# Optimization experiments

Measured on AMD Instinct MI355X. Metric: run time of the kernel, lower is better.

Reference implementation:

```python
import jax, jax.numpy as jnp
import numpy as np

B = 65536
PEP, TCR, D, FF = 384, 480, 128, 512
H1, H2, OUT = 128, 64, 1
EPS = 1e-5


def _ln(x, g, b):
    mu = jnp.mean(x, axis=-1, keepdims=True)
    var = jnp.mean((x - mu) ** 2, axis=-1, keepdims=True)
    return (x - mu) * jax.lax.rsqrt(var + EPS) * g + b


def _bn(x, g, b):
    # training-mode BatchNorm1d: batch-wide stats, biased variance
    mu = jnp.mean(x, axis=0, keepdims=True)
    var = jnp.mean((x - mu) ** 2, axis=0, keepdims=True)
    return (x - mu) * jax.lax.rsqrt(var + EPS) * g + b


def setup_inputs() -> dict:
    key = jax.random.key(0)
    ks = iter(jax.random.split(key, 40))

    def w(shape, fan):
        s = float(np.sqrt(6.0 / fan))
        return jax.random.uniform(next(ks), shape, jnp.float32, -s, s)

    inp = {
        "x": jax.random.normal(next(ks), (B, PEP + TCR), jnp.float32),
        "w_pep": w((D, PEP), PEP + D), "b_pep": jnp.zeros(D),
        "w_tcr": w((D, TCR), TCR + D), "b_tcr": jnp.zeros(D),
        "wv_p2t": w((D, D), 2 * D), "bv_p2t": jnp.zeros(D),
        "wo_p2t": w((D, D), 2 * D), "bo_p2t": jnp.zeros(D),
        "wv_t2p": w((D, D), 2 * D), "bv_t2p": jnp.zeros(D),
        "wo_t2p": w((D, D), 2 * D), "bo_t2p": jnp.zeros(D),
        "ln_g1p": jnp.ones(D), "ln_b1p": jnp.zeros(D),
        "ln_g2p": jnp.ones(D), "ln_b2p": jnp.zeros(D),
        "ln_g1t": jnp.ones(D), "ln_b1t": jnp.zeros(D),
        "ln_g2t": jnp.ones(D), "ln_b2t": jnp.zeros(D),
        "ffn_w1p": w((FF, D), D + FF), "ffn_b1p": jnp.zeros(FF),
        "ffn_w2p": w((D, FF), D + FF), "ffn_b2p": jnp.zeros(D),
        "ffn_w1t": w((FF, D), D + FF), "ffn_b1t": jnp.zeros(FF),
        "ffn_w2t": w((D, FF), D + FF), "ffn_b2t": jnp.zeros(D),
        "w_h1": w((H1, 2 * D), 2 * D + H1), "b_h1": jnp.zeros(H1),
        "bn1_g": jnp.ones(H1), "bn1_b": jnp.zeros(H1),
        "w_h2": w((H2, H1), H1 + H2), "b_h2": jnp.zeros(H2),
        "bn2_g": jnp.ones(H2), "bn2_b": jnp.zeros(H2),
        "w_out": w((OUT, H2), H2 + OUT), "b_out": jnp.zeros(OUT),
    }
    return inp


def reference(x, w_pep, b_pep, w_tcr, b_tcr,
              wv_p2t, bv_p2t, wo_p2t, bo_p2t,
              wv_t2p, bv_t2p, wo_t2p, bo_t2p,
              ln_g1p, ln_b1p, ln_g2p, ln_b2p,
              ln_g1t, ln_b1t, ln_g2t, ln_b2t,
              ffn_w1p, ffn_b1p, ffn_w2p, ffn_b2p,
              ffn_w1t, ffn_b1t, ffn_w2t, ffn_b2t,
              w_h1, b_h1, bn1_g, bn1_b,
              w_h2, b_h2, bn2_g, bn2_b,
              w_out, b_out):
    pep = x[:, :PEP] @ w_pep.T + b_pep   # (B, 128)
    tcr = x[:, PEP:] @ w_tcr.T + b_tcr   # (B, 128)

    # MHA with seq_len=1: softmax over single key == 1 exactly,
    # so attention output = out_proj(v_proj(key/value input)).
    pa = (tcr @ wv_p2t.T + bv_p2t) @ wo_p2t.T + bo_p2t
    pa = _ln(pep + pa, ln_g1p, ln_b1p)
    h = jax.nn.gelu(pa @ ffn_w1p.T + ffn_b1p, approximate=False)
    pa = _ln(pa + h @ ffn_w2p.T + ffn_b2p, ln_g2p, ln_b2p)

    ta = (pep @ wv_t2p.T + bv_t2p) @ wo_t2p.T + bo_t2p
    ta = _ln(tcr + ta, ln_g1t, ln_b1t)
    h = jax.nn.gelu(ta @ ffn_w1t.T + ffn_b1t, approximate=False)
    ta = _ln(ta + h @ ffn_w2t.T + ffn_b2t, ln_g2t, ln_b2t)

    combined = jnp.concatenate([pa, ta], axis=1)  # (B, 256)
    h1 = jax.nn.gelu(_bn(combined @ w_h1.T + b_h1, bn1_g, bn1_b), approximate=False)
    h2 = jax.nn.gelu(_bn(h1 @ w_h2.T + b_h2, bn2_g, bn2_b), approximate=False)
    return h2 @ w_out.T + b_out  # (B, 1)
```

## Files before the change

### kernel.cpp

```cpp
#include <hip/hip_runtime.h>
#include <hip/hip_bf16.h>
#include <math.h>


typedef __attribute__((ext_vector_type(8))) __bf16 bf16x8;
typedef __attribute__((ext_vector_type(8))) short s16x8;
typedef __attribute__((ext_vector_type(4))) float f32x4;

union S8U { s16x8 s; bf16x8 b; };

__device__ __forceinline__ short f2b(float f) {
  union { float f; unsigned u; } v; v.f = f;
  unsigned r = v.u + 0x7fffu + ((v.u >> 16) & 1u);
  return (short)(r >> 16);
}
__device__ __forceinline__ float b2f(short s) {
  union { unsigned u; float f; } v; v.u = ((unsigned)(unsigned short)s) << 16;
  return v.f;
}
__device__ __forceinline__ float gelu_f(float x) {
  return 0.5f * x * (1.0f + erff(x * 0.7071067811865475f));
}

template<int NTS>
__device__ __forceinline__ void mfma_step(const short* __restrict__ Abuf, int lda, int kkA,
                                          const short* __restrict__ W, int ldw, int kw,
                                          int colbase, int l16, int q,
                                          f32x4 (&acc)[4][NTS]) {
  S8U a[4];
#pragma unroll
  for (int mt = 0; mt < 4; ++mt)
    a[mt].s = *(const s16x8*)(Abuf + (16 * mt + l16) * lda + kkA + 8 * q);
#pragma unroll
  for (int nt = 0; nt < NTS; ++nt) {
    S8U b;
    b.s = *(const s16x8*)(W + (size_t)(colbase + 16 * nt + l16) * ldw + kw + 8 * q);
#pragma unroll
    for (int mt = 0; mt < 4; ++mt)
      acc[mt][nt] = __builtin_amdgcn_mfma_f32_16x16x32_bf16(a[mt].b, b.b, acc[mt][nt], 0, 0, 0);
  }
}

template<int NTS>
__device__ __forceinline__ void zero_acc(f32x4 (&acc)[4][NTS]) {
  f32x4 z = {0.f, 0.f, 0.f, 0.f};
#pragma unroll
  for (int mt = 0; mt < 4; ++mt)
#pragma unroll
    for (int nt = 0; nt < NTS; ++nt) acc[mt][nt] = z;
}

__device__ __forceinline__ void epi_bias_store(f32x4 (&acc)[4][2], const float* __restrict__ bias,
                                               short* dst, int w, int l16, int q, bool do_gelu) {
#pragma unroll
  for (int nt = 0; nt < 2; ++nt) {
    int col = 32 * w + 16 * nt + l16;
    float bb = bias[col];
#pragma unroll
    for (int mt = 0; mt < 4; ++mt)
#pragma unroll
      for (int r = 0; r < 4; ++r) {
        int row = 16 * mt + 4 * q + r;
        float v = acc[mt][nt][r] + bb;
        if (do_gelu) v = gelu_f(v);
        dst[row * 136 + col] = f2b(v);
      }
  }
}

__device__ __forceinline__ void epi_res_ln(f32x4 (&acc)[4][2], const float* __restrict__ bias,
                                           const short* resbuf,
                                           const float* __restrict__ g, const float* __restrict__ bta,
                                           short* dst, float (*lnp)[4][2], float (*murs)[2],
                                           int w, int l16, int q, int tid) {
#pragma unroll
  for (int nt = 0; nt < 2; ++nt) {
    int col = 32 * w + 16 * nt + l16;
    float bb = bias[col];
#pragma unroll
    for (int mt = 0; mt < 4; ++mt)
#pragma unroll
      for (int r = 0; r < 4; ++r) {
        int row = 16 * mt + 4 * q + r;
        acc[mt][nt][r] += bb + b2f(resbuf[row * 136 + col]);
      }
  }
#pragma unroll
  for (int mt = 0; mt < 4; ++mt) {
#pragma unroll
    for (int r = 0; r < 4; ++r) {
      float v0 = acc[mt][0][r], v1 = acc[mt][1][r];
      float s = v0 + v1;
      float sq = v0 * v0 + v1 * v1;
#pragma unroll
      for (int off = 1; off < 16; off <<= 1) {
        s += __shfl_xor(s, off);
        sq += __shfl_xor(sq, off);
      }
      if (l16 == 0) {
        int row = 16 * mt + 4 * q + r;
        lnp[row][w][0] = s;
        lnp[row][w][1] = sq;
      }
    }
  }
  __syncthreads();
  if (tid < 64) {
    float s = lnp[tid][0][0] + lnp[tid][1][0] + lnp[tid][2][0] + lnp[tid][3][0];
    float sq = lnp[tid][0][1] + lnp[tid][1][1] + lnp[tid][2][1] + lnp[tid][3][1];
    float mu = s * (1.0f / 128.0f);
    float var = sq * (1.0f / 128.0f) - mu * mu;
    murs[tid][0] = mu;
    murs[tid][1] = rsqrtf(var + 1e-5f);
  }
  __syncthreads();
#pragma unroll
  for (int nt = 0; nt < 2; ++nt) {
    int col = 32 * w + 16 * nt + l16;
    float gg = g[col], b2 = bta[col];
#pragma unroll
    for (int mt = 0; mt < 4; ++mt)
#pragma unroll
      for (int r = 0; r < 4; ++r) {
        int row = 16 * mt + 4 * q + r;
        float v = (acc[mt][nt][r] - murs[row][0]) * murs[row][1] * gg + b2;
        dst[row * 136 + col] = f2b(v);
      }
  }
}

__device__ __forceinline__ void ffn_block(const short* __restrict__ w1, const short* __restrict__ w2,
                                          const float* __restrict__ b1, const float* __restrict__ b2,
                                          const float* __restrict__ g, const float* __restrict__ bta,
                                          short* act, short* H,
                                          float (*lnp)[4][2], float (*murs)[2],
                                          int w, int l16, int q, int tid) {
  f32x4 acc2[4][2];
  zero_acc(acc2);
  for (int c = 0; c < 4; ++c) {
    f32x4 acch[4][2];
    zero_acc(acch);
#pragma unroll
    for (int kk = 0; kk < 4; ++kk)
      mfma_step<2>(act, 136, 32 * kk, w1, 128, 32 * kk, c * 128 + 32 * w, l16, q, acch);
#pragma unroll
    for (int nt = 0; nt < 2; ++nt) {
      int lcol = 32 * w + 16 * nt + l16;
      float bb = b1[c * 128 + lcol];
#pragma unroll
      for (int mt = 0; mt < 4; ++mt)
#pragma unroll
        for (int r = 0; r < 4; ++r)
          H[(16 * mt + 4 * q + r) * 136 + lcol] = f2b(gelu_f(acch[mt][nt][r] + bb));
    }
    __syncthreads();
#pragma unroll
    for (int kk = 0; kk < 4; ++kk)
      mfma_step<2>(H, 136, 32 * kk, w2, 512, c * 128 + 32 * kk, 32 * w, l16, q, acc2);
    __syncthreads();
  }
  epi_res_ln(acc2, b2, act, g, bta, act, lnp, murs, w, l16, q, tid);
}

struct K1Args {
  const float* x;
  const short *wpep, *wtcr, *wvp, *wop, *wvt, *wot, *w1p, *w2p, *w1t, *w2t, *wh1;
  const float *bpep, *btcr, *bvp, *bop, *bvt, *bot;
  const float *g1p, *e1p, *g2p, *e2p, *g1t, *e1t, *g2t, *e2t;
  const float *b1p, *b2p, *b1t, *b2t, *bh1;
  float *sum1, *sq1;
  short* h1;
};

__global__ __launch_bounds__(256, 2) void k1_main(K1Args A) {
  __shared__ __align__(16) short smem[4 * 64 * 136 + 2 * 64 * 40];
  short* U = smem;
  short* V = U + 64 * 136;
  short* T = V + 64 * 136;
  short* H = T + 64 * 136;
  short* S = H + 64 * 136;
  float (*lnp)[4][2] = (float (*)[4][2])(void*)S;
  float (*murs)[2] = (float (*)[2])(void*)(S + 1024);

  const int tid = threadIdx.x;
  const int w = tid >> 6;
  const int lane = tid & 63;
  const int l16 = lane & 15;
  const int q = lane >> 4;
  const size_t row0 = (size_t)blockIdx.x * 64;

  auto stage = [&](int kbase, short* Sb) {
    int r = tid >> 2, c8 = (tid & 3) * 8;
    const float* p = A.x + (row0 + r) * 864 + kbase + c8;
    float4 f0 = *(const float4*)p;
    float4 f1 = *(const float4*)(p + 4);
    s16x8 o;
    o[0] = f2b(f0.x); o[1] = f2b(f0.y); o[2] = f2b(f0.z); o[3] = f2b(f0.w);
    o[4] = f2b(f1.x); o[5] = f2b(f1.y); o[6] = f2b(f1.z); o[7] = f2b(f1.w);
    *(s16x8*)(Sb + r * 40 + c8) = o;
  };

  f32x4 acc[4][2];

  zero_acc(acc);
  for (int t = 0; t < 12; ++t) {
    stage(32 * t, S + (t & 1) * (64 * 40));
    __syncthreads();
    mfma_step<2>(S + (t & 1) * (64 * 40), 40, 0, A.wpep, 384, 32 * t, 32 * w, l16, q, acc);
  }
  epi_bias_store(acc, A.bpep, U, w, l16, q, false);

  zero_acc(acc);
  for (int t = 0; t < 15; ++t) {
    stage(384 + 32 * t, S + (t & 1) * (64 * 40));
    __syncthreads();
    mfma_step<2>(S + (t & 1) * (64 * 40), 40, 0, A.wtcr, 480, 32 * t, 32 * w, l16, q, acc);
  }
  epi_bias_store(acc, A.btcr, V, w, l16, q, false);
  __syncthreads();

  zero_acc(acc);
#pragma unroll
  for (int kk = 0; kk < 4; ++kk)
    mfma_step<2>(V, 136, 32 * kk, A.wvp, 128, 32 * kk, 32 * w, l16, q, acc);
  epi_bias_store(acc, A.bvp, T, w, l16, q, false);

  zero_acc(acc);
#pragma unroll
  for (int kk = 0; kk < 4; ++kk)
    mfma_step<2>(U, 136, 32 * kk, A.wvt, 128, 32 * kk, 32 * w, l16, q, acc);
  epi_bias_store(acc, A.bvt, H, w, l16, q, false);
  __syncthreads();

  zero_acc(acc);
#pragma unroll
  for (int kk = 0; kk < 4; ++kk)
    mfma_step<2>(T, 136, 32 * kk, A.wop, 128, 32 * kk, 32 * w, l16, q, acc);
  epi_res_ln(acc, A.bop, U, A.g1p, A.e1p, U, lnp, murs, w, l16, q, tid);

  zero_acc(acc);
#pragma unroll
  for (int kk = 0; kk < 4; ++kk)
    mfma_step<2>(H, 136, 32 * kk, A.wot, 128, 32 * kk, 32 * w, l16, q, acc);
  epi_res_ln(acc, A.bot, V, A.g1t, A.e1t, V, lnp, murs, w, l16, q, tid);

  ffn_block(A.w1p, A.w2p, A.b1p, A.b2p, A.g2p, A.e2p, U, H, lnp, murs, w, l16, q, tid);
  ffn_block(A.w1t, A.w2t, A.b1t, A.b2t, A.g2t, A.e2t, V, H, lnp, murs, w, l16, q, tid);
  __syncthreads();

  zero_acc(acc);
#pragma unroll
  for (int s = 0; s < 8; ++s)
    mfma_step<2>((s < 4) ? U : V, 136, 32 * (s & 3), A.wh1, 256, 32 * s, 32 * w, l16, q, acc);
#pragma unroll
  for (int nt = 0; nt < 2; ++nt) {
    int col = 32 * w + 16 * nt + l16;
    float bb = A.bh1[col];
    float s = 0.f, sq = 0.f;
#pragma unroll
    for (int mt = 0; mt < 4; ++mt)
#pragma unroll
      for (int r = 0; r < 4; ++r) {
        float v = acc[mt][nt][r] + bb;
        s += v; sq += v * v;
        A.h1[(row0 + 16 * mt + 4 * q + r) * 128 + col] = f2b(v);
      }
    s += __shfl_xor(s, 16); sq += __shfl_xor(sq, 16);
    s += __shfl_xor(s, 32); sq += __shfl_xor(sq, 32);
    if (q == 0) {
      atomicAdd(&A.sum1[col], s);
      atomicAdd(&A.sq1[col], sq);
    }
  }
}

struct K2Args {
  const short* h1;
  const short* wh2;
  const float *bh2, *bn1g, *bn1b;
  const float *sum1, *sq1;
  float *sum2, *sq2;
  short* h2;
};

__global__ __launch_bounds__(256) void k2_main(K2Args A) {
  __shared__ __align__(16) short S2[64 * 136];
  __shared__ float s1[128], t1[128];
  const int tid = threadIdx.x;
  const int w = tid >> 6, lane = tid & 63, l16 = lane & 15, q = lane >> 4;
  const size_t row0 = (size_t)blockIdx.x * 64;

  if (tid < 128) {
    float su = A.sum1[tid], sq = A.sq1[tid];
    float mu = su * (1.0f / 65536.0f);
    float var = sq * (1.0f / 65536.0f) - mu * mu;
    float sc = A.bn1g[tid] * rsqrtf(var + 1e-5f);
    s1[tid] = sc;
    t1[tid] = A.bn1b[tid] - mu * sc;
  }
  __syncthreads();
  {
    int r = tid >> 2;
#pragma unroll
    for (int j = 0; j < 4; ++j) {
      int c = (tid & 3) * 32 + j * 8;
      s16x8 hv = *(const s16x8*)(A.h1 + (row0 + r) * 128 + c);
      s16x8 o;
#pragma unroll
      for (int i = 0; i < 8; ++i) {
        float f = b2f(hv[i]);
        f = gelu_f(f * s1[c + i] + t1[c + i]);
        o[i] = f2b(f);
      }
      *(s16x8*)(S2 + r * 136 + c) = o;
    }
  }
  __syncthreads();
  f32x4 acc[4][1];
  zero_acc(acc);
#pragma unroll
  for (int kk = 0; kk < 4; ++kk)
    mfma_step<1>(S2, 136, 32 * kk, A.wh2, 128, 32 * kk, 16 * w, l16, q, acc);
  int col = 16 * w + l16;
  float bb = A.bh2[col];
  float s = 0.f, sq = 0.f;
#pragma unroll
  for (int mt = 0; mt < 4; ++mt)
#pragma unroll
    for (int r = 0; r < 4; ++r) {
      float v = acc[mt][0][r] + bb;
      s += v; sq += v * v;
      A.h2[(row0 + 16 * mt + 4 * q + r) * 64 + col] = f2b(v);
    }
  s += __shfl_xor(s, 16); sq += __shfl_xor(sq, 16);
  s += __shfl_xor(s, 32); sq += __shfl_xor(sq, 32);
  if (q == 0) {
    atomicAdd(&A.sum2[col], s);
    atomicAdd(&A.sq2[col], sq);
  }
}

struct K3Args {
  const short* h2;
  const float *bn2g, *bn2b;
  const float *sum2, *sq2;
  const float *wout, *bout;
  float* out;
};

__global__ __launch_bounds__(256) void k3_main(K3Args A) {
  __shared__ float s2[64], t2[64], wo[64];
  const int tid = threadIdx.x;
  if (tid < 64) {
    float su = A.sum2[tid], sq = A.sq2[tid];
    float mu = su * (1.0f / 65536.0f);
    float var = sq * (1.0f / 65536.0f) - mu * mu;
    float sc = A.bn2g[tid] * rsqrtf(var + 1e-5f);
    s2[tid] = sc;
    t2[tid] = A.bn2b[tid] - mu * sc;
    wo[tid] = A.wout[tid];
  }
  __syncthreads();
  size_t row = (size_t)blockIdx.x * 32 + (tid >> 3);
  int c0 = (tid & 7) * 8;
  s16x8 hv = *(const s16x8*)(A.h2 + row * 64 + c0);
  float s = 0.f;
#pragma unroll
  for (int i = 0; i < 8; ++i) {
    float f = b2f(hv[i]);
    f = gelu_f(f * s2[c0 + i] + t2[c0 + i]);
    s += f * wo[c0 + i];
  }
  s += __shfl_xor(s, 1); s += __shfl_xor(s, 2); s += __shfl_xor(s, 4);
  if ((tid & 7) == 0) A.out[row] = s + A.bout[0];
}

struct CvtArgs {
  const float* src[12];
  short* dst;
  float* stats;
};

__global__ __launch_bounds__(256) void k0_setup(CvtArgs A) {
  const int cum[13] = {0, 49152, 110592, 126976, 143360, 159744, 176128,
                       241664, 307200, 372736, 438272, 471040, 479232};
  int b = blockIdx.x;
  if (b == 0) {
    A.stats[threadIdx.x] = 0.0f;
    if (threadIdx.x < 128) A.stats[256 + threadIdx.x] = 0.0f;
  }
  int base = b * 1024;
  int seg = 0;
#pragma unroll
  for (int t = 1; t < 12; ++t) seg += (base >= cum[t]) ? 1 : 0;
  const float* s = A.src[seg];
  int loc = base - cum[seg] + threadIdx.x * 4;
  float4 f = *(const float4*)(s + loc);
  int di = base + threadIdx.x * 4;
  A.dst[di + 0] = f2b(f.x);
  A.dst[di + 1] = f2b(f.y);
  A.dst[di + 2] = f2b(f.z);
  A.dst[di + 3] = f2b(f.w);
}

extern "C" void kernel_launch(void* const* d_in, const int* in_sizes, int n_in,
                              void* d_out, int out_size, void* d_ws, size_t ws_size,
                              hipStream_t stream) {
  (void)in_sizes; (void)n_in; (void)out_size; (void)ws_size;
  const float* x = (const float*)d_in[0];
  char* ws = (char*)d_ws;
  short* wb = (short*)ws;
  enum { O_PEP = 0, O_TCR = 49152, O_VP2T = 110592, O_OP2T = 126976,
         O_VT2P = 143360, O_OT2P = 159744, O_W1P = 176128, O_W2P = 241664,
         O_W1T = 307200, O_W2T = 372736, O_H1 = 438272, O_H2 = 471040 };
  float* stats = (float*)(ws + 958464);
  short* h1_pre = (short*)(ws + 960000);
  short* h2_pre = (short*)(ws + 17737216);

  CvtArgs ca;
  ca.src[0]  = (const float*)d_in[1];
  ca.src[1]  = (const float*)d_in[3];
  ca.src[2]  = (const float*)d_in[5];
  ca.src[3]  = (const float*)d_in[7];
  ca.src[4]  = (const float*)d_in[9];
  ca.src[5]  = (const float*)d_in[11];
  ca.src[6]  = (const float*)d_in[21];
  ca.src[7]  = (const float*)d_in[23];
  ca.src[8]  = (const float*)d_in[25];
  ca.src[9]  = (const float*)d_in[27];
  ca.src[10] = (const float*)d_in[29];
  ca.src[11] = (const float*)d_in[33];
  ca.dst = wb;
  ca.stats = stats;
  k0_setup<<<468, 256, 0, stream>>>(ca);

  K1Args a1;
  a1.x = x;
  a1.wpep = wb + O_PEP;  a1.wtcr = wb + O_TCR;
  a1.wvp = wb + O_VP2T;  a1.wop = wb + O_OP2T;
  a1.wvt = wb + O_VT2P;  a1.wot = wb + O_OT2P;
  a1.w1p = wb + O_W1P;   a1.w2p = wb + O_W2P;
  a1.w1t = wb + O_W1T;   a1.w2t = wb + O_W2T;
  a1.wh1 = wb + O_H1;
  a1.bpep = (const float*)d_in[2];
  a1.btcr = (const float*)d_in[4];
  a1.bvp = (const float*)d_in[6];
  a1.bop = (const float*)d_in[8];
  a1.bvt = (const float*)d_in[10];
  a1.bot = (const float*)d_in[12];
  a1.g1p = (const float*)d_in[13];  a1.e1p = (const float*)d_in[14];
  a1.g2p = (const float*)d_in[15];  a1.e2p = (const float*)d_in[16];
  a1.g1t = (const float*)d_in[17];  a1.e1t = (const float*)d_in[18];
  a1.g2t = (const float*)d_in[19];  a1.e2t = (const float*)d_in[20];
  a1.b1p = (const float*)d_in[22];
  a1.b2p = (const float*)d_in[24];
  a1.b1t = (const float*)d_in[26];
  a1.b2t = (const float*)d_in[28];
  a1.bh1 = (const float*)d_in[30];
  a1.sum1 = stats;
  a1.sq1 = stats + 128;
  a1.h1 = h1_pre;
  k1_main<<<1024, 256, 0, stream>>>(a1);

  K2Args a2;
  a2.h1 = h1_pre;
  a2.wh2 = wb + O_H2;
  a2.bh2 = (const float*)d_in[34];
  a2.bn1g = (const float*)d_in[31];
  a2.bn1b = (const float*)d_in[32];
  a2.sum1 = stats;
  a2.sq1 = stats + 128;
  a2.sum2 = stats + 256;
  a2.sq2 = stats + 320;
  a2.h2 = h2_pre;
  k2_main<<<1024, 256, 0, stream>>>(a2);

  K3Args a3;
  a3.h2 = h2_pre;
  a3.bn2g = (const float*)d_in[35];
  a3.bn2b = (const float*)d_in[36];
  a3.sum2 = stats + 256;
  a3.sq2 = stats + 320;
  a3.wout = (const float*)d_in[37];
  a3.bout = (const float*)d_in[38];
  a3.out = (float*)d_out;
  k3_main<<<2048, 256, 0, stream>>>(a3);
}
```

Measured before the change: 596.9 us.

## Fold attention V/O projections into one matrix and pipeline input staging

The setup kernel now precomputes Wo·Wv and Wo·bv+bo for each attention direction, which removes one 128x128 GEMM per direction from the main kernel. The main kernel's input staging is restructured to stream 64-column tiles with register prefetch across the combined pep/tcr loop, halving the barrier count. Shared memory is shrunk by dropping two activation buffers, and launch bounds are raised to 3 blocks per CU. The fused weight is rounded to bf16 after composition, which slightly changes numerics compared with two separate bf16 GEMMs.

```diff
diff --git a/kernel.cpp b/kernel.cpp
--- a/kernel.cpp
+++ b/kernel.cpp
@@ -1,5 +1,4 @@
 #include <hip/hip_runtime.h>
-#include <hip/hip_bf16.h>
 #include <math.h>
 
 
@@ -160,27 +159,29 @@
     __syncthreads();
   }
   epi_res_ln(acc2, b2, act, g, bta, act, lnp, murs, w, l16, q, tid);
+  __syncthreads();
 }
 
 struct K1Args {
   const float* x;
-  const short *wpep, *wtcr, *wvp, *wop, *wvt, *wot, *w1p, *w2p, *w1t, *w2t, *wh1;
-  const float *bpep, *btcr, *bvp, *bop, *bvt, *bot;
+  const short *wpep, *wtcr, *wcp, *wct, *w1p, *w2p, *w1t, *w2t, *wh1;
+  const float *bpep, *btcr, *bcp, *bct;
   const float *g1p, *e1p, *g2p, *e2p, *g1t, *e1t, *g2t, *e2t;
   const float *b1p, *b2p, *b1t, *b2t, *bh1;
   float *sum1, *sq1;
   short* h1;
 };
 
-__global__ __launch_bounds__(256, 2) void k1_main(K1Args A) {
-  __shared__ __align__(16) short smem[4 * 64 * 136 + 2 * 64 * 40];
+__global__ __launch_bounds__(256, 3) void k1_main(K1Args A) {
+  __shared__ __align__(16) short smem[2 * 64 * 136 + 2 * 64 * 72];
   short* U = smem;
   short* V = U + 64 * 136;
-  short* T = V + 64 * 136;
-  short* H = T + 64 * 136;
-  short* S = H + 64 * 136;
-  float (*lnp)[4][2] = (float (*)[4][2])(void*)S;
-  float (*murs)[2] = (float (*)[2])(void*)(S + 1024);
+  short* Rst = V + 64 * 136;
+  short* R0 = Rst;
+  short* R1 = Rst + 64 * 72;
+  short* Hb = Rst;
+  float (*lnp)[4][2] = (float (*)[4][2])(void*)(Rst + 7936);
+  float (*murs)[2] = (float (*)[2])(void*)(Rst + 8960);
 
   const int tid = threadIdx.x;
   const int w = tid >> 6;
@@ -189,69 +190,83 @@
   const int q = lane >> 4;
   const size_t row0 = (size_t)blockIdx.x * 64;
 
-  auto stage = [&](int kbase, short* Sb) {
-    int r = tid >> 2, c8 = (tid & 3) * 8;
-    const float* p = A.x + (row0 + r) * 864 + kbase + c8;
-    float4 f0 = *(const float4*)p;
-    float4 f1 = *(const float4*)(p + 4);
-    s16x8 o;
-    o[0] = f2b(f0.x); o[1] = f2b(f0.y); o[2] = f2b(f0.z); o[3] = f2b(f0.w);
-    o[4] = f2b(f1.x); o[5] = f2b(f1.y); o[6] = f2b(f1.z); o[7] = f2b(f1.w);
-    *(s16x8*)(Sb + r * 40 + c8) = o;
+  const int r_st = tid >> 2;
+  const float* xrow = A.x + (row0 + r_st) * 864;
+
+  float4 pf0, pf1, pf2, pf3;
+  auto issue64 = [&](int kb) {
+    const float* p = xrow + kb + (tid & 3) * 16;
+    pf0 = *(const float4*)(p);
+    pf1 = *(const float4*)(p + 4);
+    pf2 = *(const float4*)(p + 8);
+    pf3 = *(const float4*)(p + 12);
   };
-
-  f32x4 acc[4][2];
-
-  zero_acc(acc);
-  for (int t = 0; t < 12; ++t) {
-    stage(32 * t, S + (t & 1) * (64 * 40));
+  auto write64 = [&](short* Sb) {
+    int c = (tid & 3) * 16;
+    s16x8 o0, o1;
+    o0[0] = f2b(pf0.x); o0[1] = f2b(pf0.y); o0[2] = f2b(pf0.z); o0[3] = f2b(pf0.w);
+    o0[4] = f2b(pf1.x); o0[5] = f2b(pf1.y); o0[6] = f2b(pf1.z); o0[7] = f2b(pf1.w);
+    o1[0] = f2b(pf2.x); o1[1] = f2b(pf2.y); o1[2] = f2b(pf2.z); o1[3] = f2b(pf2.w);
+    o1[4] = f2b(pf3.x); o1[5] = f2b(pf3.y); o1[6] = f2b(pf3.z); o1[7] = f2b(pf3.w);
+    *(s16x8*)(Sb + r_st * 72 + c) = o0;
+    *(s16x8*)(Sb + r_st * 72 + c + 8) = o1;
+  };
+  auto issue32 = [&](int kb) {
+    const float* p = xrow + kb + (tid & 3) * 8;
+    pf0 = *(const float4*)(p);
+    pf1 = *(const float4*)(p + 4);
+  };
+  auto write32 = [&](short* Sb) {
+    int c = (tid & 3) * 8;
+    s16x8 o0;
+    o0[0] = f2b(pf0.x); o0[1] = f2b(pf0.y); o0[2] = f2b(pf0.z); o0[3] = f2b(pf0.w);
+    o0[4] = f2b(pf1.x); o0[5] = f2b(pf1.y); o0[6] = f2b(pf1.z); o0[7] = f2b(pf1.w);
+    *(s16x8*)(Sb + r_st * 72 + c) = o0;
+  };
+
+  f32x4 accP[4][2], accT[4][2];
+  zero_acc(accP); zero_acc(accT);
+
+  issue64(0); write64(R0);
+  __syncthreads();
+  for (int t = 0; t < 14; ++t) {
+    short* cur = (t & 1) ? R1 : R0;
+    short* nxt = (t & 1) ? R0 : R1;
+    if (t < 13) { if (t == 12) issue32(832); else issue64(64 * (t + 1)); }
+    if (t < 6) {
+      mfma_step<2>(cur, 72, 0,  A.wpep, 384, 64 * t,      32 * w, l16, q, accP);
+      mfma_step<2>(cur, 72, 32, A.wpep, 384, 64 * t + 32, 32 * w, l16, q, accP);
+    } else if (t < 13) {
+      mfma_step<2>(cur, 72, 0,  A.wtcr, 480, 64 * (t - 6),      32 * w, l16, q, accT);
+      mfma_step<2>(cur, 72, 32, A.wtcr, 480, 64 * (t - 6) + 32, 32 * w, l16, q, accT);
+    } else {
+      mfma_step<2>(cur, 72, 0,  A.wtcr, 480, 448, 32 * w, l16, q, accT);
+    }
+    if (t < 13) { if (t == 12) write32(nxt); else write64(nxt); }
     __syncthreads();
-    mfma_step<2>(S + (t & 1) * (64 * 40), 40, 0, A.wpep, 384, 32 * t, 32 * w, l16, q, acc);
-  }
-  epi_bias_store(acc, A.bpep, U, w, l16, q, false);
-
-  zero_acc(acc);
-  for (int t = 0; t < 15; ++t) {
-    stage(384 + 32 * t, S + (t & 1) * (64 * 40));
-    __syncthreads();
-    mfma_step<2>(S + (t & 1) * (64 * 40), 40, 0, A.wtcr, 480, 32 * t, 32 * w, l16, q, acc);
-  }
-  epi_bias_store(acc, A.btcr, V, w, l16, q, false);
-  __syncthreads();
-
-  zero_acc(acc);
+  }
+  epi_bias_store(accP, A.bpep, U, w, l16, q, false);
+  epi_bias_store(accT, A.btcr, V, w, l16, q, false);
+  __syncthreads();
+
+  zero_acc(accP); zero_acc(accT);
 #pragma unroll
   for (int kk = 0; kk < 4; ++kk)
-    mfma_step<2>(V, 136, 32 * kk, A.wvp, 128, 32 * kk, 32 * w, l16, q, acc);
-  epi_bias_store(acc, A.bvp, T, w, l16, q, false);
-
-  zero_acc(acc);
+    mfma_step<2>(V, 136, 32 * kk, A.wcp, 128, 32 * kk, 32 * w, l16, q, accP);
 #pragma unroll
   for (int kk = 0; kk < 4; ++kk)
-    mfma_step<2>(U, 136, 32 * kk, A.wvt, 128, 32 * kk, 32 * w, l16, q, acc);
-  epi_bias_store(acc, A.bvt, H, w, l16, q, false);
-  __syncthreads();
-
-  zero_acc(acc);
-#pragma unroll
-  for (int kk = 0; kk < 4; ++kk)
-    mfma_step<2>(T, 136, 32 * kk, A.wop, 128, 32 * kk, 32 * w, l16, q, acc);
-  epi_res_ln(acc, A.bop, U, A.g1p, A.e1p, U, lnp, murs, w, l16, q, tid);
-
-  zero_acc(acc);
-#pragma unroll
-  for (int kk = 0; kk < 4; ++kk)
-    mfma_step<2>(H, 136, 32 * kk, A.wot, 128, 32 * kk, 32 * w, l16, q, acc);
-  epi_res_ln(acc, A.bot, V, A.g1t, A.e1t, V, lnp, murs, w, l16, q, tid);
-
-  ffn_block(A.w1p, A.w2p, A.b1p, A.b2p, A.g2p, A.e2p, U, H, lnp, murs, w, l16, q, tid);
-  ffn_block(A.w1t, A.w2t, A.b1t, A.b2t, A.g2t, A.e2t, V, H, lnp, murs, w, l16, q, tid);
-  __syncthreads();
-
-  zero_acc(acc);
+    mfma_step<2>(U, 136, 32 * kk, A.wct, 128, 32 * kk, 32 * w, l16, q, accT);
+  epi_res_ln(accP, A.bcp, U, A.g1p, A.e1p, U, lnp, murs, w, l16, q, tid);
+  epi_res_ln(accT, A.bct, V, A.g1t, A.e1t, V, lnp, murs, w, l16, q, tid);
+  __syncthreads();
+
+  ffn_block(A.w1p, A.w2p, A.b1p, A.b2p, A.g2p, A.e2p, U, Hb, lnp, murs, w, l16, q, tid);
+  ffn_block(A.w1t, A.w2t, A.b1t, A.b2t, A.g2t, A.e2t, V, Hb, lnp, murs, w, l16, q, tid);
+
+  zero_acc(accP);
 #pragma unroll
   for (int s = 0; s < 8; ++s)
-    mfma_step<2>((s < 4) ? U : V, 136, 32 * (s & 3), A.wh1, 256, 32 * s, 32 * w, l16, q, acc);
+    mfma_step<2>((s < 4) ? U : V, 136, 32 * (s & 3), A.wh1, 256, 32 * s, 32 * w, l16, q, accP);
 #pragma unroll
   for (int nt = 0; nt < 2; ++nt) {
     int col = 32 * w + 16 * nt + l16;
@@ -261,7 +276,7 @@
     for (int mt = 0; mt < 4; ++mt)
 #pragma unroll
       for (int r = 0; r < 4; ++r) {
-        float v = acc[mt][nt][r] + bb;
+        float v = accP[mt][nt][r] + bb;
         s += v; sq += v * v;
         A.h1[(row0 + 16 * mt + 4 * q + r) * 128 + col] = f2b(v);
       }
@@ -376,27 +391,52 @@
 }
 
 struct CvtArgs {
-  const float* src[12];
+  const float* src[8];
   short* dst;
   float* stats;
+  const float *wv[2], *wo[2], *bv[2], *bo[2];
+  short* wc[2];
+  float* bc[2];
 };
 
 __global__ __launch_bounds__(256) void k0_setup(CvtArgs A) {
-  const int cum[13] = {0, 49152, 110592, 126976, 143360, 159744, 176128,
-                       241664, 307200, 372736, 438272, 471040, 479232};
   int b = blockIdx.x;
+  const int tid = threadIdx.x;
+  if (b >= 404) {
+    int b2 = b - 404, pair = b2 >> 4, part = b2 & 15;
+    const float* wv = A.wv[pair];
+    const float* wo = A.wo[pair];
+#pragma unroll
+    for (int i = 0; i < 4; ++i) {
+      int idx = part * 1024 + i * 256 + tid;
+      int o = idx >> 7, k = idx & 127;
+      const float* worow = wo + o * 128;
+      float acc = 0.f;
+#pragma unroll 4
+      for (int j = 0; j < 128; ++j) acc += worow[j] * wv[j * 128 + k];
+      A.wc[pair][idx] = f2b(acc);
+    }
+    if (part == 0 && tid < 128) {
+      const float* bvp = A.bv[pair];
+      float acc = A.bo[pair][tid];
+      for (int j = 0; j < 128; ++j) acc += wo[tid * 128 + j] * bvp[j];
+      A.bc[pair][tid] = acc;
+    }
+    return;
+  }
+  const int st[8] = {0, 49152, 176128, 241664, 307200, 372736, 438272, 471040};
   if (b == 0) {
-    A.stats[threadIdx.x] = 0.0f;
-    if (threadIdx.x < 128) A.stats[256 + threadIdx.x] = 0.0f;
-  }
-  int base = b * 1024;
+    A.stats[tid] = 0.0f;
+    if (tid < 128) A.stats[256 + tid] = 0.0f;
+  }
+  int dstbase = b * 1024 + ((b >= 108) ? 65536 : 0);
   int seg = 0;
 #pragma unroll
-  for (int t = 1; t < 12; ++t) seg += (base >= cum[t]) ? 1 : 0;
+  for (int t = 1; t < 8; ++t) seg += (dstbase >= st[t]) ? 1 : 0;
   const float* s = A.src[seg];
-  int loc = base - cum[seg] + threadIdx.x * 4;
+  int loc = dstbase - st[seg] + tid * 4;
   float4 f = *(const float4*)(s + loc);
-  int di = base + threadIdx.x * 4;
+  int di = dstbase + tid * 4;
   A.dst[di + 0] = f2b(f.x);
   A.dst[di + 1] = f2b(f.y);
   A.dst[di + 2] = f2b(f.z);
@@ -410,44 +450,44 @@
   const float* x = (const float*)d_in[0];
   char* ws = (char*)d_ws;
   short* wb = (short*)ws;
-  enum { O_PEP = 0, O_TCR = 49152, O_VP2T = 110592, O_OP2T = 126976,
-         O_VT2P = 143360, O_OT2P = 159744, O_W1P = 176128, O_W2P = 241664,
+  enum { O_PEP = 0, O_TCR = 49152, O_WCP = 110592, O_BCF = 126976,
+         O_WCT = 143360, O_W1P = 176128, O_W2P = 241664,
          O_W1T = 307200, O_W2T = 372736, O_H1 = 438272, O_H2 = 471040 };
   float* stats = (float*)(ws + 958464);
   short* h1_pre = (short*)(ws + 960000);
   short* h2_pre = (short*)(ws + 17737216);
+  float* bcomp = (float*)(ws + (size_t)O_BCF * 2);
 
   CvtArgs ca;
-  ca.src[0]  = (const float*)d_in[1];
-  ca.src[1]  = (const float*)d_in[3];
-  ca.src[2]  = (const float*)d_in[5];
-  ca.src[3]  = (const float*)d_in[7];
-  ca.src[4]  = (const float*)d_in[9];
-  ca.src[5]  = (const float*)d_in[11];
-  ca.src[6]  = (const float*)d_in[21];
-  ca.src[7]  = (const float*)d_in[23];
-  ca.src[8]  = (const float*)d_in[25];
-  ca.src[9]  = (const float*)d_in[27];
-  ca.src[10] = (const float*)d_in[29];
-  ca.src[11] = (const float*)d_in[33];
+  ca.src[0] = (const float*)d_in[1];
+  ca.src[1] = (const float*)d_in[3];
+  ca.src[2] = (const float*)d_in[21];
+  ca.src[3] = (const float*)d_in[23];
+  ca.src[4] = (const float*)d_in[25];
+  ca.src[5] = (const float*)d_in[27];
+  ca.src[6] = (const float*)d_in[29];
+  ca.src[7] = (const float*)d_in[33];
   ca.dst = wb;
   ca.stats = stats;
-  k0_setup<<<468, 256, 0, stream>>>(ca);
+  ca.wv[0] = (const float*)d_in[5];   ca.bv[0] = (const float*)d_in[6];
+  ca.wo[0] = (const float*)d_in[7];   ca.bo[0] = (const float*)d_in[8];
+  ca.wv[1] = (const float*)d_in[9];   ca.bv[1] = (const float*)d_in[10];
+  ca.wo[1] = (const float*)d_in[11];  ca.bo[1] = (const float*)d_in[12];
+  ca.wc[0] = wb + O_WCP;  ca.wc[1] = wb + O_WCT;
+  ca.bc[0] = bcomp;       ca.bc[1] = bcomp + 128;
+  k0_setup<<<436, 256, 0, stream>>>(ca);
 
   K1Args a1;
   a1.x = x;
   a1.wpep = wb + O_PEP;  a1.wtcr = wb + O_TCR;
-  a1.wvp = wb + O_VP2T;  a1.wop = wb + O_OP2T;
-  a1.wvt = wb + O_VT2P;  a1.wot = wb + O_OT2P;
+  a1.wcp = wb + O_WCP;   a1.wct = wb + O_WCT;
   a1.w1p = wb + O_W1P;   a1.w2p = wb + O_W2P;
   a1.w1t = wb + O_W1T;   a1.w2t = wb + O_W2T;
   a1.wh1 = wb + O_H1;
   a1.bpep = (const float*)d_in[2];
   a1.btcr = (const float*)d_in[4];
-  a1.bvp = (const float*)d_in[6];
-  a1.bop = (const float*)d_in[8];
-  a1.bvt = (const float*)d_in[10];
-  a1.bot = (const float*)d_in[12];
+  a1.bcp = bcomp;
+  a1.bct = bcomp + 128;
   a1.g1p = (const float*)d_in[13];  a1.e1p = (const float*)d_in[14];
   a1.g2p = (const float*)d_in[15];  a1.e2p = (const float*)d_in[16];
   a1.g1t = (const float*)d_in[17];  a1.e1t = (const float*)d_in[18];
```

Result: slower. 611.6 us (+2.5%).
